# Kernel optimization log

Hardware: AMD Instinct MI355X
Metric: run time of the kernel (lower is better)

The kernel has to match this reference:

```python
import jax, jax.numpy as jnp
import numpy as np

B, T, C = 2, 4096, 768
N_HEAD = 12
HEAD_DIM = C // N_HEAD


def setup_inputs() -> dict:
    key = jax.random.key(0)
    k1, k2, k3, k4, k5 = jax.random.split(key, 5)
    scale = 1.0 / np.sqrt(C)
    x = jax.random.normal(k1, (B, T, C), dtype=jnp.float32)
    # weights stored as [in, out] (transpose of torch Linear weight)
    W_attn = jax.random.normal(k2, (C, 3 * C), dtype=jnp.float32) * scale
    b_attn = jax.random.normal(k3, (3 * C,), dtype=jnp.float32) * 0.01
    W_proj = jax.random.normal(k4, (C, C), dtype=jnp.float32) * scale
    b_proj = jax.random.normal(k5, (C,), dtype=jnp.float32) * 0.01
    return {"x": x, "W_attn": W_attn, "b_attn": b_attn, "W_proj": W_proj, "b_proj": b_proj}


def reference(x, W_attn, b_attn, W_proj, b_proj):
    Bq, Tq, Cq = x.shape
    qkv = x @ W_attn + b_attn                      # [B, T, 3C]
    q, k, v = jnp.split(qkv, 3, axis=-1)           # each [B, T, C]

    def heads(t):
        return t.reshape(Bq, Tq, N_HEAD, HEAD_DIM).transpose(0, 2, 1, 3)  # [B, H, T, D]

    q, k, v = heads(q), heads(k), heads(v)
    att = jnp.einsum('bhqd,bhkd->bhqk', q, k) * (1.0 / np.sqrt(HEAD_DIM))  # [B, H, T, T]
    causal = jnp.tril(jnp.ones((Tq, Tq), dtype=bool))                      # [T, T]
    att = jnp.where(causal[None, None], att, jnp.finfo(att.dtype).min)
    att = jax.nn.softmax(att, axis=-1)
    y = jnp.einsum('bhqk,bhkd->bhqd', att, v)      # [B, H, T, D]
    y = y.transpose(0, 2, 1, 3).reshape(Bq, Tq, Cq)
    return y @ W_proj + b_proj
```

## Files before the change

kernel.cpp:

```cpp
#include <hip/hip_runtime.h>


#define TSEQ   4096
#define NHEAD  12
#define CDIM   768
#define C3     2304
#define BT_TOT 8192

typedef __bf16 bf16x8 __attribute__((ext_vector_type(8)));
typedef __bf16 bf16x2 __attribute__((ext_vector_type(2)));
typedef float  f32x4  __attribute__((ext_vector_type(4)));
typedef unsigned int u32x4 __attribute__((ext_vector_type(4)));

__device__ __forceinline__ unsigned short f2bf(float f) {
  unsigned int u = __builtin_bit_cast(unsigned int, f);
  u += 0x7FFFu + ((u >> 16) & 1u);
  return (unsigned short)(u >> 16);
}

__device__ __forceinline__ unsigned int pack2bf(float a, float b) {
  bf16x2 v = {(__bf16)a, (__bf16)b};
  return __builtin_bit_cast(unsigned int, v);
}

__device__ __forceinline__ f32x4 mfma16(bf16x8 a, bf16x8 b, f32x4 c) {
  return __builtin_amdgcn_mfma_f32_16x16x32_bf16(a, b, c, 0, 0, 0);
}

typedef const __attribute__((address_space(1))) void* gas_ptr;
typedef __attribute__((address_space(3))) void* las_ptr;


#define PREP_CAST_BLOCKS  6144
#define PREP_WA_BLOCKS    1728
#define PREP_WP_BLOCKS     576

__global__ __launch_bounds__(256) void prep_kernel(
    const float* __restrict__ x, unsigned short* __restrict__ xb,
    const float* __restrict__ W_attn, unsigned short* __restrict__ WaT,
    const float* __restrict__ W_proj, unsigned short* __restrict__ WpT) {
  const int bk = blockIdx.x;
  if (bk < PREP_CAST_BLOCKS) {
    int i = (bk * 256 + threadIdx.x) * 4;
    float4 v = *(const float4*)(x + i);
    ushort4 u;
    u.x = f2bf(v.x); u.y = f2bf(v.y); u.z = f2bf(v.z); u.w = f2bf(v.w);
    *(ushort4*)(xb + i) = u;
    return;
  }
  __shared__ float tile[32][33];
  const float* src;
  unsigned short* dst;
  int K, N, n0, k0;
  if (bk < PREP_CAST_BLOCKS + PREP_WA_BLOCKS) {
    const int j = bk - PREP_CAST_BLOCKS;
    src = W_attn; dst = WaT; K = CDIM; N = C3;
    n0 = (j % 72) * 32; k0 = (j / 72) * 32;
  } else {
    const int j = bk - (PREP_CAST_BLOCKS + PREP_WA_BLOCKS);
    src = W_proj; dst = WpT; K = CDIM; N = CDIM;
    n0 = (j % 24) * 32; k0 = (j / 24) * 32;
  }
  const int tx = threadIdx.x & 31, ty = threadIdx.x >> 5;
#pragma unroll
  for (int i = 0; i < 4; ++i)
    tile[ty + i * 8][tx] = src[(size_t)(k0 + ty + i * 8) * N + n0 + tx];
  __syncthreads();
#pragma unroll
  for (int i = 0; i < 4; ++i)
    dst[(size_t)(n0 + ty + i * 8) * K + k0 + tx] = f2bf(tile[tx][ty + i * 8]);
}


__device__ __forceinline__ void stage_gemm(const unsigned short* __restrict__ A,
                                           const unsigned short* __restrict__ BTm,
                                           int K, int m0, int n0, int k0,
                                           unsigned short* buf, int wave,
                                           int srow, int scol) {
#pragma unroll
  for (int r = 0; r < 2; ++r) {
    const unsigned short* ga = A + (size_t)(m0 + r * 64 + srow) * K + k0 + scol;
    __builtin_amdgcn_global_load_lds((gas_ptr)ga,
        (las_ptr)(buf + r * 2048 + wave * 512), 16, 0, 0);
    const unsigned short* gb = BTm + (size_t)(n0 + r * 64 + srow) * K + k0 + scol;
    __builtin_amdgcn_global_load_lds((gas_ptr)gb,
        (las_ptr)(buf + 4096 + r * 2048 + wave * 512), 16, 0, 0);
  }
}

__device__ __forceinline__ void gemm_bt_mainloop(const unsigned short* __restrict__ A,
                                                 const unsigned short* __restrict__ BTm,
                                                 int K, int m0, int n0,
                                                 unsigned short* lds, f32x4 acc[4][4]) {
  const int tid = threadIdx.x;
  const int wave = tid >> 6, lane = tid & 63;
  const int quad = lane >> 4, l16 = lane & 15;
  const int wm = (wave >> 1) * 64, wn = (wave & 1) * 64;
  const int srow = tid >> 2;
  const int scol = (tid & 3) * 8;

  stage_gemm(A, BTm, K, m0, n0, 0, lds, wave, srow, scol);
  __syncthreads();

  int cur = 0;
  for (int k0 = 0; k0 < K; k0 += 32) {
    if (k0 + 32 < K)
      stage_gemm(A, BTm, K, m0, n0, k0 + 32, lds + (cur ^ 1) * 8192, wave, srow, scol);

    const unsigned short* buf = lds + cur * 8192;
    bf16x8 af[4], bfr[4];
#pragma unroll
    for (int i = 0; i < 4; ++i) {
      af[i]  = *(const bf16x8*)(buf + (wm + i * 16 + l16) * 32 + quad * 8);
      bfr[i] = *(const bf16x8*)(buf + 4096 + (wn + i * 16 + l16) * 32 + quad * 8);
    }
#pragma unroll
    for (int i = 0; i < 4; ++i)
#pragma unroll
      for (int j = 0; j < 4; ++j)
        acc[i][j] = mfma16(af[i], bfr[j], acc[i][j]);

    __syncthreads();
    cur ^= 1;
  }
}

__global__ __launch_bounds__(256, 4) void gemm_qkv_kernel(
    const unsigned short* __restrict__ A, const unsigned short* __restrict__ BTm,
    const float* __restrict__ bias,
    unsigned short* __restrict__ qbuf, unsigned short* __restrict__ kbuf,
    unsigned short* __restrict__ vtbuf) {
  __shared__ __align__(16) unsigned short lds[128 * 136];
  f32x4 zero = {0.f, 0.f, 0.f, 0.f};
  f32x4 acc[4][4];
#pragma unroll
  for (int i = 0; i < 4; ++i)
#pragma unroll
    for (int j = 0; j < 4; ++j) acc[i][j] = zero;

  const int m0 = blockIdx.y * 128, n0 = blockIdx.x * 128;
  gemm_bt_mainloop(A, BTm, CDIM, m0, n0, lds, acc);

  const int tid = threadIdx.x;
  const int wave = tid >> 6, lane = tid & 63;
  const int quad = lane >> 4, l16 = lane & 15;
  const int wm = (wave >> 1) * 64, wn = (wave & 1) * 64;
  const float KSCALE = 0.125f * 1.44269504088896340736f;

  const int seg = n0 / CDIM;
  const float mult = (seg == 1) ? KSCALE : 1.0f;

#pragma unroll
  for (int j = 0; j < 4; ++j) {
    const int nl = wn + j * 16 + l16;
    const float bv = bias[n0 + nl];
#pragma unroll
    for (int i = 0; i < 4; ++i) {
#pragma unroll
      for (int r = 0; r < 4; ++r) {
        const int ml = wm + i * 16 + quad * 4 + r;
        unsigned short val = f2bf((acc[i][j][r] + bv) * mult);
        if (seg < 2) lds[ml * 136 + nl] = val;
        else         lds[nl * 136 + ml] = val;
      }
    }
  }
  __syncthreads();

  const int row = tid >> 1, half = tid & 1;
  const unsigned short* src = lds + row * 136 + half * 64;
  if (seg < 2) {
    const int m = m0 + row, b = m >> 12, t = m & (TSEQ - 1);
    const int nn = (n0 - seg * CDIM) + half * 64;
    const int h = nn >> 6;
    unsigned short* base = (seg == 0) ? qbuf : kbuf;
    unsigned short* dst = base + ((size_t)(b * NHEAD + h) * TSEQ + t) * 64;
#pragma unroll
    for (int k = 0; k < 8; ++k)
      *(uint4*)(dst + k * 8) = *(const uint4*)(src + k * 8);
  } else {
    const int nn = (n0 - 2 * CDIM) + row;
    const int h = nn >> 6, d = nn & 63;
    const int b = m0 >> 12, t0 = (m0 & (TSEQ - 1)) + half * 64;
    unsigned short* dst = vtbuf + ((size_t)(b * NHEAD + h) * 64 + d) * TSEQ + t0;
#pragma unroll
    for (int k = 0; k < 8; ++k) {
      const int s0 = 32 * (k >> 2) + 4 * (k & 3);
      uint2 a = *(const uint2*)(src + s0);
      uint2 c = *(const uint2*)(src + s0 + 16);
      uint4 w = {a.x, a.y, c.x, c.y};
      *(uint4*)(dst + k * 8) = w;
    }
  }
}

__global__ __launch_bounds__(256, 4) void gemm_out_kernel(
    const unsigned short* __restrict__ A, const unsigned short* __restrict__ BTm,
    const float* __restrict__ bias, float* __restrict__ out) {
  __shared__ __align__(16) unsigned short lds[16384];
  f32x4 zero = {0.f, 0.f, 0.f, 0.f};
  f32x4 acc[4][4];
#pragma unroll
  for (int i = 0; i < 4; ++i)
#pragma unroll
    for (int j = 0; j < 4; ++j) acc[i][j] = zero;

  const int m0 = blockIdx.y * 128, n0 = blockIdx.x * 128;
  gemm_bt_mainloop(A, BTm, CDIM, m0, n0, lds, acc);

  const int tid = threadIdx.x;
  const int wave = tid >> 6, lane = tid & 63;
  const int quad = lane >> 4, l16 = lane & 15;
  const int wm = (wave >> 1) * 64, wn = (wave & 1) * 64;

#pragma unroll
  for (int j = 0; j < 4; ++j) {
    int n = n0 + wn + j * 16 + l16;
    float bv = bias[n];
#pragma unroll
    for (int i = 0; i < 4; ++i) {
#pragma unroll
      for (int r = 0; r < 4; ++r) {
        int m = m0 + wm + i * 16 + quad * 4 + r;
        out[(size_t)m * CDIM + n] = acc[i][j][r] + bv;
      }
    }
  }
}


__device__ __forceinline__ void stage_kv(const unsigned short* __restrict__ Kp,
                                         const unsigned short* __restrict__ Vp,
                                         int j0, unsigned short* kb, unsigned short* vb,
                                         int tid, int wave) {
  const int row = tid >> 3;
  const int col = ((tid & 7) ^ (row & 7)) * 8;
  __builtin_amdgcn_global_load_lds((gas_ptr)(Kp + (size_t)(j0 + row) * 64 + col),
                                   (las_ptr)(kb + wave * 512), 16, 0, 0);
  __builtin_amdgcn_global_load_lds((gas_ptr)(Vp + (size_t)row * TSEQ + j0 + col),
                                   (las_ptr)(vb + wave * 512), 16, 0, 0);
}

__device__ __forceinline__ void qk_score(const bf16x8 kf[8], const bf16x8 qf[2], f32x4 s[4]) {
  f32x4 zero = {0.f, 0.f, 0.f, 0.f};
#pragma unroll
  for (int i = 0; i < 4; ++i)
    s[i] = mfma16(kf[2 * i + 1], qf[1], mfma16(kf[2 * i], qf[0], zero));
}

template <bool MASKED>
__device__ __forceinline__ void exp_pack(const f32x4 s[4], int j0, int qabs,
                                         int l16, int quad, float& lsum, bf16x8 pf[2]) {
  unsigned int w[8];
#pragma unroll
  for (int i = 0; i < 4; ++i) {
    float p[4];
#pragma unroll
    for (int r = 0; r < 4; ++r) {
      p[r] = __builtin_amdgcn_exp2f(s[i][r]);
      if (MASKED) {
        if (j0 + i * 16 + quad * 4 + r > qabs) p[r] = 0.f;
      }
      lsum += p[r];
    }
    w[2 * i]     = pack2bf(p[0], p[1]);
    w[2 * i + 1] = pack2bf(p[2], p[3]);
  }
  u32x4 lo = {w[0], w[1], w[2], w[3]};
  u32x4 hi = {w[4], w[5], w[6], w[7]};
  pf[0] = __builtin_bit_cast(bf16x8, lo);
  pf[1] = __builtin_bit_cast(bf16x8, hi);
}

__device__ __forceinline__ void pv(const unsigned short* __restrict__ vb,
                                   int l16, int quad, int x7,
                                   const bf16x8 pf[2], f32x4 o[4]) {
#pragma unroll
  for (int dt = 0; dt < 4; ++dt) {
    const unsigned short* vr = vb + (dt * 16 + l16) * 64;
    bf16x8 v0 = *(const bf16x8*)(vr + ((quad ^ x7) * 8));
    bf16x8 v1 = *(const bf16x8*)(vr + (((4 + quad) ^ x7) * 8));
    o[dt] = mfma16(v1, pf[1], mfma16(v0, pf[0], o[dt]));
  }
}

__global__ __launch_bounds__(512, 6) void attn_kernel(const unsigned short* __restrict__ qbuf,
                                                      const unsigned short* __restrict__ kbuf,
                                                      const unsigned short* __restrict__ vtbuf,
                                                      unsigned short* __restrict__ y) {
  __shared__ __align__(16) unsigned short k_lds[2][64 * 64];
  __shared__ __align__(16) unsigned short v_lds[2][64 * 64];

  const int tid = threadIdx.x;
  const int wave = tid >> 6, lane = tid & 63;
  const int quad = lane >> 4, l16 = lane & 15;
  const int x7 = l16 & 7;

  const int bh = blockIdx.x % 24;
  const int p = blockIdx.x / 24;
  const bool isA = wave < 4;
  const int qtile = isA ? p : (63 - p);
  const int q0 = qtile * 64 + (wave & 3) * 16;

  const unsigned short* Qp = qbuf + (size_t)bh * TSEQ * 64;
  const unsigned short* Kp = kbuf + (size_t)bh * TSEQ * 64;
  const unsigned short* Vp = vtbuf + (size_t)bh * 64 * TSEQ;

  bf16x8 qf[2];
  qf[0] = *(const bf16x8*)(Qp + (size_t)(q0 + l16) * 64 + quad * 8);
  qf[1] = *(const bf16x8*)(Qp + (size_t)(q0 + l16) * 64 + 32 + quad * 8);

  f32x4 zero = {0.f, 0.f, 0.f, 0.f};
  f32x4 o[4];
#pragma unroll
  for (int dt = 0; dt < 4; ++dt) o[dt] = zero;
  float ls = 0.f;

  const int kcol0 = (quad ^ x7) * 8;
  const int ntiles = 64 - p;
  const int lasttile = isA ? p : (ntiles - 1);

  stage_kv(Kp, Vp, 0, k_lds[0], v_lds[0], tid, wave);

  for (int jt = 0; jt < ntiles; ++jt) {
    __syncthreads();
    if (jt + 1 < ntiles)
      stage_kv(Kp, Vp, (jt + 1) * 64, k_lds[(jt + 1) & 1], v_lds[(jt + 1) & 1], tid, wave);

    if (jt <= lasttile) {
      const unsigned short* kb = k_lds[jt & 1];
      const unsigned short* vb = v_lds[jt & 1];
      const int j0 = jt * 64;

      bf16x8 kf[8];
#pragma unroll
      for (int i = 0; i < 4; ++i) {
        kf[2 * i]     = *(const bf16x8*)(kb + (16 * i + l16) * 64 + kcol0);
        kf[2 * i + 1] = *(const bf16x8*)(kb + (16 * i + l16) * 64 + (kcol0 ^ 32));
      }

      f32x4 s[4];
      qk_score(kf, qf, s);

      bf16x8 pf[2];
      if (jt == lasttile) exp_pack<true>(s, j0, q0 + l16, l16, quad, ls, pf);
      else                exp_pack<false>(s, j0, q0 + l16, l16, quad, ls, pf);

      pv(vb, l16, quad, x7, pf, o);
    }
  }

  ls += __shfl_xor(ls, 16); ls += __shfl_xor(ls, 32);
  const float inv = 1.0f / ls;

  const int b = bh / NHEAD, hd = bh - b * NHEAD;
  unsigned short* yr = y + (size_t)(b * TSEQ + q0 + l16) * CDIM + hd * 64 + quad * 4;
#pragma unroll
  for (int dt = 0; dt < 4; ++dt) {
    uint2 w;
    w.x = pack2bf(o[dt][0] * inv, o[dt][1] * inv);
    w.y = pack2bf(o[dt][2] * inv, o[dt][3] * inv);
    *(uint2*)(yr + dt * 16) = w;
  }
}


extern "C" void kernel_launch(void* const* d_in, const int* in_sizes, int n_in,
                              void* d_out, int out_size, void* d_ws, size_t ws_size,
                              hipStream_t stream) {
  const float* x      = (const float*)d_in[0];
  const float* W_attn = (const float*)d_in[1];
  const float* b_attn = (const float*)d_in[2];
  const float* W_proj = (const float*)d_in[3];
  const float* b_proj = (const float*)d_in[4];
  float* out = (float*)d_out;

  unsigned short* xb    = (unsigned short*)d_ws;
  unsigned short* WaT   = xb + (size_t)BT_TOT * CDIM;
  unsigned short* WpT   = WaT + (size_t)C3 * CDIM;
  unsigned short* qbuf  = WpT + (size_t)CDIM * CDIM;
  unsigned short* kbuf  = qbuf + (size_t)2 * NHEAD * TSEQ * 64;
  unsigned short* vtbuf = kbuf + (size_t)2 * NHEAD * TSEQ * 64;
  unsigned short* ybuf  = xb;

  prep_kernel<<<PREP_CAST_BLOCKS + PREP_WA_BLOCKS + PREP_WP_BLOCKS, 256, 0, stream>>>(
      x, xb, W_attn, WaT, W_proj, WpT);
  gemm_qkv_kernel<<<dim3(C3 / 128, BT_TOT / 128), 256, 0, stream>>>(xb, WaT, b_attn,
                                                                    qbuf, kbuf, vtbuf);
  attn_kernel<<<dim3(24 * 32), 512, 0, stream>>>(qbuf, kbuf, vtbuf, ybuf);
  gemm_out_kernel<<<dim3(CDIM / 128, BT_TOT / 128), 256, 0, stream>>>(ybuf, WpT, b_proj, out);
}
```

Measured before the change: 222.8 us.

## Triple-buffer GEMM mainloop with explicit vmcnt waits and single barrier per step

The shared GEMM mainloop moves from double to triple buffering in LDS. It keeps two K-tiles of async global-to-LDS loads in flight and uses explicit s_waitcnt vmcnt values plus raw s_barrier instead of a full __syncthreads each iteration. The aim is to hide global load latency behind the MFMA work in the QKV and output projection GEMMs. In exchange LDS per block grows to 48KB and the launch-bounds occupancy hint drops from 4 to 3. The hand-coded waitcnt encodings also carry some correctness risk.

```diff
diff --git a/kernel.cpp b/kernel.cpp
--- a/kernel.cpp
+++ b/kernel.cpp
@@ -29,6 +29,10 @@
 
 typedef const __attribute__((address_space(1))) void* gas_ptr;
 typedef __attribute__((address_space(3))) void* las_ptr;
+
+#define WAIT_VM4() __builtin_amdgcn_s_waitcnt(0x3F74)
+#define WAIT_VM0() __builtin_amdgcn_s_waitcnt(0x3F70)
+#define SBAR()     __builtin_amdgcn_sched_barrier(0)
 
 
 #define PREP_CAST_BLOCKS  6144
@@ -99,15 +103,25 @@
   const int srow = tid >> 2;
   const int scol = (tid & 3) * 8;
 
-  stage_gemm(A, BTm, K, m0, n0, 0, lds, wave, srow, scol);
-  __syncthreads();
-
-  int cur = 0;
-  for (int k0 = 0; k0 < K; k0 += 32) {
-    if (k0 + 32 < K)
-      stage_gemm(A, BTm, K, m0, n0, k0 + 32, lds + (cur ^ 1) * 8192, wave, srow, scol);
-
-    const unsigned short* buf = lds + cur * 8192;
+  const int nt = K / 32;
+  stage_gemm(A, BTm, K, m0, n0, 0,  lds,        wave, srow, scol);
+  stage_gemm(A, BTm, K, m0, n0, 32, lds + 8192, wave, srow, scol);
+  WAIT_VM4();
+  SBAR();
+  __builtin_amdgcn_s_barrier();
+  SBAR();
+
+  for (int t = 0; t < nt; ++t) {
+    if (t + 2 < nt) {
+      stage_gemm(A, BTm, K, m0, n0, (t + 2) * 32, lds + ((t + 2) % 3) * 8192,
+                 wave, srow, scol);
+      WAIT_VM4();
+    } else {
+      WAIT_VM0();
+    }
+    SBAR();
+
+    const unsigned short* buf = lds + (t % 3) * 8192;
     bf16x8 af[4], bfr[4];
 #pragma unroll
     for (int i = 0; i < 4; ++i) {
@@ -120,17 +134,21 @@
       for (int j = 0; j < 4; ++j)
         acc[i][j] = mfma16(af[i], bfr[j], acc[i][j]);
 
-    __syncthreads();
-    cur ^= 1;
-  }
-}
-
-__global__ __launch_bounds__(256, 4) void gemm_qkv_kernel(
+    if (t + 1 < nt) {
+      SBAR();
+      __builtin_amdgcn_s_barrier();
+      SBAR();
+    }
+  }
+  __syncthreads();
+}
+
+__global__ __launch_bounds__(256, 3) void gemm_qkv_kernel(
     const unsigned short* __restrict__ A, const unsigned short* __restrict__ BTm,
     const float* __restrict__ bias,
     unsigned short* __restrict__ qbuf, unsigned short* __restrict__ kbuf,
     unsigned short* __restrict__ vtbuf) {
-  __shared__ __align__(16) unsigned short lds[128 * 136];
+  __shared__ __align__(16) unsigned short lds[3 * 8192];
   f32x4 zero = {0.f, 0.f, 0.f, 0.f};
   f32x4 acc[4][4];
 #pragma unroll
@@ -194,10 +212,10 @@
   }
 }
 
-__global__ __launch_bounds__(256, 4) void gemm_out_kernel(
+__global__ __launch_bounds__(256, 3) void gemm_out_kernel(
     const unsigned short* __restrict__ A, const unsigned short* __restrict__ BTm,
     const float* __restrict__ bias, float* __restrict__ out) {
-  __shared__ __align__(16) unsigned short lds[16384];
+  __shared__ __align__(16) unsigned short lds[3 * 8192];
   f32x4 zero = {0.f, 0.f, 0.f, 0.f};
   f32x4 acc[4][4];
 #pragma unroll
```

After: 221.0 us (median of 2 runs). About the same (-0.8%).
